# Kernel optimization log

Measured on AMD Instinct MI355X. Metric: run time of the kernel, lower is better.

Reference implementation:

```python
import jax, jax.numpy as jnp
import numpy as np

# config: nsql-350M-like, 8 layers
L, D, H, HD, FF, V, RD, MP = 8, 1024, 16, 64, 4096, 51200, 32, 4


def setup_inputs() -> dict:
    key = jax.random.key(0)
    ks = jax.random.split(key, 8)
    B, S = 1, 1024
    s = 0.02
    return {
        'idx': jax.random.randint(ks[0], (B, S), 0, V),
        'input_pos': jnp.arange(S),
        'emb': jax.random.normal(ks[1], (V, D)) * s,
        'Wqkv': jax.random.normal(ks[2], (L, 3 * D, D)) * s,
        'Wo': jax.random.normal(ks[3], (L, D, D)) * s,
        'ln1_w': jnp.ones((L, D)), 'ln1_b': jnp.zeros((L, D)),
        'fc_in_w': jax.random.normal(ks[4], (L, FF, D)) * s,
        'fc_in_b': jnp.zeros((L, FF)),
        'fc_out_w': jax.random.normal(ks[5], (L, D, FF)) * s,
        'fc_out_b': jnp.zeros((L, D)),
        'lnf_w': jnp.ones((D,)), 'lnf_b': jnp.zeros((D,)),
        'lm_w': jax.random.normal(ks[6], (V, D)) * s,
        'lm_b': jnp.zeros((V,)),
    }


def _layer_norm(x, w, b, eps=1e-5):
    mu = jnp.mean(x, axis=-1, keepdims=True)
    var = jnp.var(x, axis=-1, keepdims=True)
    return (x - mu) * jax.lax.rsqrt(var + eps) * w + b


def _new_gelu(x):
    # transformers NewGELUActivation == tanh-approx gelu
    return jax.nn.gelu(x, approximate=True)


def _sincos(input_pos):
    # create_sinusoidal_positions over rotary_dim, gathered at input_pos
    inv_freq = 1.0 / (10000.0 ** (jnp.arange(0, RD, 2, dtype=jnp.float32) / RD))
    ang = input_pos.astype(jnp.float32)[:, None] * inv_freq          # [S, RD/2]
    # repeat_interleave(..., 2, dim=-1) -> interleaved sin/cos, shape [1,S,1,RD]
    sin = jnp.repeat(jnp.sin(ang), 2, axis=-1)[None, :, None, :]
    cos = jnp.repeat(jnp.cos(ang), 2, axis=-1)[None, :, None, :]
    return sin, cos


def _rotary(x, sin, cos):
    # x: [B,S,H,HD]; GPT-J interleaved rotary on first RD dims
    xr, xp = x[..., :RD], x[..., RD:]
    x1, x2 = xr[..., ::2], xr[..., 1::2]
    rot = jnp.stack((-x2, x1), axis=-1).reshape(xr.shape)  # rotate_every_two
    return jnp.concatenate([xr * cos + rot * sin, xp], axis=-1)


def reference(idx, input_pos, emb, Wqkv, Wo, ln1_w, ln1_b, fc_in_w, fc_in_b,
              fc_out_w, fc_out_b, lnf_w, lnf_b, lm_w, lm_b):
    B, S = idx.shape
    x = emb[idx]                                        # [B,S,D]
    sin, cos = _sincos(input_pos)
    causal = jnp.tril(jnp.ones((S, S), dtype=bool))
    neg = jnp.finfo(x.dtype).min
    ld = D // MP

    def split_heads(t):
        # CodeGen _split_heads with mp_num=4: [B,S,MP,ld] -> [B,S,H,HD]
        return t.reshape(B, S, MP, H // MP, HD).reshape(B, S, H, HD)

    for l in range(L):
        h = _layer_norm(x, ln1_w[l], ln1_b[l])
        qkv = (h @ Wqkv[l].T).reshape(B, S, MP, 3 * ld)
        q, v, k = qkv[..., :ld], qkv[..., ld:2 * ld], qkv[..., 2 * ld:]  # q,v,k order!
        q = _rotary(split_heads(q), sin, cos)
        k = _rotary(split_heads(k), sin, cos)
        vh = split_heads(v)
        q, k, vh = (jnp.transpose(t, (0, 2, 1, 3)) for t in (q, k, vh))  # [B,H,S,HD]
        scores = jnp.einsum('bhqd,bhkd->bhqk', q, k) / jnp.sqrt(jnp.asarray(HD, x.dtype))
        scores = jnp.where(causal, scores, neg)
        att = jax.nn.softmax(scores, axis=-1)
        y = jnp.einsum('bhqk,bhkd->bhqd', att, vh)
        y = jnp.transpose(y, (0, 2, 1, 3)).reshape(B, S, D)
        attn_out = y @ Wo[l].T
        mlp = _new_gelu(h @ fc_in_w[l].T + fc_in_b[l]) @ fc_out_w[l].T + fc_out_b[l]
        x = attn_out + mlp + x                          # parallel block + residual

    x = _layer_norm(x, lnf_w, lnf_b)
    return x @ lm_w.T + lm_b                            # [B,S,V]
```

## Files before the change

kernel.cpp:

```cpp
#include <hip/hip_runtime.h>

#define SQ 1024
#define DIM 1024
#define NH 16
#define HDIM 64
#define FFD 4096
#define NV 51200
#define NL 8
#define LDBUF 5120
#define WELEMS ((long)(3 * DIM + DIM + FFD + FFD) * DIM)

typedef __bf16 bf16x8 __attribute__((ext_vector_type(8)));
typedef float f32x4 __attribute__((ext_vector_type(4)));

__device__ __forceinline__ unsigned short f2bf(float f) {
    union { float f; unsigned int i; } v; v.f = f;
    unsigned int r = v.i + 0x7fffu + ((v.i >> 16) & 1u);
    return (unsigned short)(r >> 16);
}
__device__ __forceinline__ float gelu_tanh(float x) {
    float x3 = x * x * x;
    return 0.5f * x * (1.0f + tanhf(0.79788456080286535588f * (x + 0.044715f * x3)));
}
__device__ __forceinline__ void cvt8(const float* __restrict__ s, unsigned short* __restrict__ d, long i) {
    float4 a = *reinterpret_cast<const float4*>(s + i);
    float4 b = *reinterpret_cast<const float4*>(s + i + 4);
    bf16x8 w;
    w[0] = (__bf16)a.x; w[1] = (__bf16)a.y; w[2] = (__bf16)a.z; w[3] = (__bf16)a.w;
    w[4] = (__bf16)b.x; w[5] = (__bf16)b.y; w[6] = (__bf16)b.z; w[7] = (__bf16)b.w;
    *reinterpret_cast<bf16x8*>(d + i) = w;
}

#define GLD16(gp, lp) __builtin_amdgcn_global_load_lds( \
    (__attribute__((address_space(1))) void*)(gp), \
    (__attribute__((address_space(3))) void*)(lp), 16, 0, 0)
#define VMCNT0 asm volatile("s_waitcnt vmcnt(0)" ::: "memory")

__global__ void cvt4_kernel(const float* __restrict__ w0, const float* __restrict__ w1,
                            const float* __restrict__ w2, const float* __restrict__ w3,
                            unsigned short* __restrict__ dst) {
    const int b = blockIdx.x;
    const float* s; long off; unsigned short* d;
    if (b < 1536)      { s = w0; d = dst;                      off = (long)b * 2048; }
    else if (b < 2048) { s = w1; d = dst + (long)3072 * 1024;  off = (long)(b - 1536) * 2048; }
    else if (b < 4096) { s = w2; d = dst + (long)4096 * 1024;  off = (long)(b - 2048) * 2048; }
    else               { s = w3; d = dst + (long)8192 * 1024;  off = (long)(b - 4096) * 2048; }
    cvt8(s, d, off + threadIdx.x * 8);
}
__global__ void cvt_kernel(const float* __restrict__ src, unsigned short* __restrict__ dst) {
    cvt8(src, dst, ((long)blockIdx.x * 256 + threadIdx.x) * 8);
}

__global__ void sincos_kernel(const int* __restrict__ pos, float2* __restrict__ sc) {
    const int t = blockIdx.x * 256 + threadIdx.x;
    if (t >= SQ * 16) return;
    const int s = t >> 4, i = t & 15;
    const float ang = (float)pos[s] * powf(10000.0f, -(float)i / 16.0f);
    sc[t] = make_float2(sinf(ang), cosf(ang));
}

__global__ void embed_kernel(const int* __restrict__ idx, const float* __restrict__ emb,
                             float* __restrict__ x) {
    const int s = blockIdx.x;
    const int d = threadIdx.x * 4;
    const int row = idx[s];
    *reinterpret_cast<float4*>(x + (long)s * DIM + d) =
        *reinterpret_cast<const float4*>(emb + (long)row * DIM + d);
}

template <bool RED>
__global__ __launch_bounds__(256) void ln_kernel(float* __restrict__ x,
                                                 const float* __restrict__ part,
                                                 const float* __restrict__ w,
                                                 const float* __restrict__ b,
                                                 unsigned short* __restrict__ out) {
    __shared__ float red[8];
    const int s = blockIdx.x, tid = threadIdx.x;
    const long fidx = (long)s * 256 + tid;
    float4 v = reinterpret_cast<const float4*>(x)[fidx];
    if (RED) {
        #pragma unroll
        for (int z = 0; z < 4; z++) {
            float4 p = reinterpret_cast<const float4*>(part + (long)z * SQ * DIM)[fidx];
            v.x += p.x; v.y += p.y; v.z += p.z; v.w += p.w;
        }
        reinterpret_cast<float4*>(x)[fidx] = v;
    }
    float sum = v.x + v.y + v.z + v.w;
    float sq = v.x * v.x + v.y * v.y + v.z * v.z + v.w * v.w;
    #pragma unroll
    for (int off = 32; off; off >>= 1) { sum += __shfl_xor(sum, off); sq += __shfl_xor(sq, off); }
    const int wid = tid >> 6, lane = tid & 63;
    if (lane == 0) { red[wid * 2] = sum; red[wid * 2 + 1] = sq; }
    __syncthreads();
    sum = red[0] + red[2] + red[4] + red[6];
    sq  = red[1] + red[3] + red[5] + red[7];
    const float mu = sum * (1.0f / DIM);
    const float var = sq * (1.0f / DIM) - mu * mu;
    const float rstd = rsqrtf(var + 1e-5f);
    const int d = tid * 4;
    float vv[4] = {v.x, v.y, v.z, v.w};
    ushort4 o;
    unsigned short* op = (unsigned short*)&o;
    #pragma unroll
    for (int j = 0; j < 4; j++)
        op[j] = f2bf((vv[j] - mu) * rstd * w[d + j] + b[d + j]);
    *reinterpret_cast<ushort4*>(out + (long)s * DIM + d) = o;
}

__global__ __launch_bounds__(256) void gemm_qkv_fcin(const unsigned short* __restrict__ A,
                                                     const unsigned short* __restrict__ B1,
                                                     const unsigned short* __restrict__ B2,
                                                     const float* __restrict__ bias,
                                                     unsigned short* __restrict__ ffout,
                                                     const float2* __restrict__ sc,
                                                     unsigned short* __restrict__ qt,
                                                     unsigned short* __restrict__ kt,
                                                     unsigned short* __restrict__ vt,
                                                     const float* __restrict__ lmsrc,
                                                     unsigned short* __restrict__ lmdst) {
    __shared__ __align__(16) unsigned short As[2][128 * 64];
    __shared__ __align__(16) unsigned short Bs[2][128 * 64];
    const int tid = threadIdx.x;
    if (blockIdx.x >= 448) {
        if (lmdst) {
            const int cb = (int)blockIdx.x - 448;
            const long stride = (long)((int)gridDim.x - 448) * 256;
            const long nlmv = (long)(NV / NL) * DIM / 8;
            for (long i = (long)cb * 256 + tid; i < nlmv; i += stride) cvt8(lmsrc, lmdst, i * 8);
        }
        return;
    }
    const int sb = (blockIdx.x & 7) * 56 + (blockIdx.x >> 3);
    const int mb = sb & 7, nb = sb >> 3;
    const int m0 = mb * 128, n0 = nb * 128;
    const int lane = tid & 63, wid = tid >> 6;
    const int l15 = lane & 15, lhi = lane >> 4;
    const int wr = wid >> 1, wc = wid & 1;
    const int sw = l15 & 7;

    const unsigned short* Bbase = B1;
    int nloc = n0;
    if (nb >= 24) { Bbase = B2; nloc = n0 - 3072; }

    f32x4 acc[4][4];
    #pragma unroll
    for (int i = 0; i < 4; i++)
        #pragma unroll
        for (int j = 0; j < 4; j++) acc[i][j] = (f32x4){0.f, 0.f, 0.f, 0.f};

    const int wbase = (tid & ~63) * 8;

    auto stage = [&](int buf, int kt_) {
        const int k0 = kt_ << 6;
        #pragma unroll
        for (int i = 0; i < 4; i++) {
            const int e = (i * 256 + tid) * 8;
            const int r = e >> 6;
            const int cs = (((e >> 3) & 7) ^ (r & 7)) * 8;
            GLD16(A + (long)(m0 + r) * DIM + k0 + cs, &As[buf][i * 2048 + wbase]);
        }
        #pragma unroll
        for (int i = 0; i < 4; i++) {
            const int e = (i * 256 + tid) * 8;
            const int r = e >> 6;
            const int cs = (((e >> 3) & 7) ^ (r & 7)) * 8;
            GLD16(Bbase + (long)(nloc + r) * 1024 + k0 + cs, &Bs[buf][i * 2048 + wbase]);
        }
    };
    auto compute = [&](int buf) {
        #pragma unroll
        for (int ks = 0; ks < 2; ks++) {
            bf16x8 af[4], bfr[4];
            #pragma unroll
            for (int mf = 0; mf < 4; mf++)
                af[mf] = *reinterpret_cast<const bf16x8*>(
                    &As[buf][(wr * 64 + mf * 16 + l15) * 64 + ((ks * 4 + lhi) ^ sw) * 8]);
            #pragma unroll
            for (int nf = 0; nf < 4; nf++)
                bfr[nf] = *reinterpret_cast<const bf16x8*>(
                    &Bs[buf][(wc * 64 + nf * 16 + l15) * 64 + ((ks * 4 + lhi) ^ sw) * 8]);
            #pragma unroll
            for (int mf = 0; mf < 4; mf++)
                #pragma unroll
                for (int nf = 0; nf < 4; nf++)
                    acc[mf][nf] = __builtin_amdgcn_mfma_f32_16x16x32_bf16(af[mf], bfr[nf], acc[mf][nf], 0, 0, 0);
        }
    };

    int cur = 0;
    stage(0, 0);
    VMCNT0; __syncthreads();
    for (int kt_ = 0; kt_ < 16; kt_++) {
        if (kt_ + 1 < 16) stage(cur ^ 1, kt_ + 1);
        compute(cur);
        if (kt_ + 1 < 16) { VMCNT0; __syncthreads(); cur ^= 1; }
    }

    if (nb < 24) {
        #pragma unroll
        for (int nf = 0; nf < 4; nf++) {
            const int col = n0 + wc * 64 + nf * 16 + l15;
            const int g = col / 768;
            const int r768 = col - g * 768;
            const int sec = r768 >> 8;
            const int off = r768 & 255;
            const int h = g * 4 + (off >> 6);
            const int d = off & 63;
            const bool isrot = (d < 32);
            const int dodd = d & 1;
            #pragma unroll
            for (int mf = 0; mf < 4; mf++) {
                #pragma unroll
                for (int j = 0; j < 4; j++) {
                    const int row = m0 + wr * 64 + mf * 16 + lhi * 4 + j;
                    float v = acc[mf][nf][j];
                    const float pv = __shfl_xor(v, 1);
                    float outv = v;
                    if (isrot && sec != 1) {
                        const float2 scv = sc[row * 16 + (d >> 1)];
                        outv = dodd ? (v * scv.y + pv * scv.x)
                                    : (v * scv.y - pv * scv.x);
                    }
                    if (sec == 0)      qt[((long)(h * SQ + row)) * HDIM + d] = f2bf(outv);
                    else if (sec == 2) kt[((long)(h * SQ + row)) * HDIM + d] = f2bf(outv);
                    else               vt[(long)h * (HDIM * SQ) + (long)d * SQ + row] = f2bf(outv);
                }
            }
        }
    } else {
        #pragma unroll
        for (int nf = 0; nf < 4; nf++) {
            const int col = n0 + wc * 64 + nf * 16 + l15;
            #pragma unroll
            for (int mf = 0; mf < 4; mf++) {
                #pragma unroll
                for (int j = 0; j < 4; j++) {
                    const int row = m0 + wr * 64 + mf * 16 + lhi * 4 + j;
                    float v = gelu_tanh(acc[mf][nf][j] + bias[col - 3072]);
                    ffout[(long)row * LDBUF + (col - 3072)] = f2bf(v);
                }
            }
        }
    }
}

__global__ __launch_bounds__(256) void attn_fcout(const unsigned short* __restrict__ qt,
                                                  const unsigned short* __restrict__ kt,
                                                  const unsigned short* __restrict__ vt,
                                                  unsigned short* __restrict__ buf,
                                                  const unsigned short* __restrict__ fcw,
                                                  const float* __restrict__ fcb,
                                                  float* __restrict__ parts,
                                                  const float* __restrict__ nw0,
                                                  const float* __restrict__ nw1,
                                                  const float* __restrict__ nw2,
                                                  const float* __restrict__ nw3,
                                                  unsigned short* __restrict__ nd) {
    __shared__ __align__(16) unsigned short smem[32768];
    const int tid = threadIdx.x, lane = tid & 63, wid = tid >> 6;
    const int l15 = lane & 15, lhi = lane >> 4;
    const int sw = l15 & 7;
    const int wbase = (tid & ~63) * 8;

    if (blockIdx.x < 256) {
        unsigned short* Ks0 = smem;
        unsigned short* Vs0 = smem + 8192;
        unsigned short* Psw = smem + 16384 + wid * 1024;
        const int h = blockIdx.x & 15;
        const int qb = 15 - ((int)blockIdx.x >> 4);
        const int q0 = qb * 64 + wid * 16;

        bf16x8 aq[2];
        {
            const unsigned short* qp = qt + ((long)(h * SQ + q0 + l15)) * HDIM;
            aq[0] = *reinterpret_cast<const bf16x8*>(qp + lhi * 8);
            aq[1] = *reinterpret_cast<const bf16x8*>(qp + 32 + lhi * 8);
        }
        f32x4 o[4];
        #pragma unroll
        for (int nf = 0; nf < 4; nf++) o[nf] = (f32x4){0.f, 0.f, 0.f, 0.f};
        float mrow[4] = {-1e30f, -1e30f, -1e30f, -1e30f};
        float lrow[4] = {0.f, 0.f, 0.f, 0.f};

        auto stageKV = [&](int b, int kv0) {
            #pragma unroll
            for (int i = 0; i < 2; i++) {
                const int e = (i * 256 + tid) * 8;
                const int r = e >> 6;
                const int cs = (((e >> 3) & 7) ^ (r & 7)) * 8;
                GLD16(kt + ((long)(h * SQ + kv0 + r)) * HDIM + cs, Ks0 + b * 4096 + i * 2048 + wbase);
                GLD16(vt + (long)h * (HDIM * SQ) + (long)r * SQ + kv0 + cs, Vs0 + b * 4096 + i * 2048 + wbase);
            }
        };

        int cur = 0;
        stageKV(0, 0);
        VMCNT0; __syncthreads();
        for (int kvt = 0; kvt <= qb; kvt++) {
            const int kv0 = kvt * 64;
            if (kvt < qb) stageKV(cur ^ 1, kv0 + 64);

            f32x4 sa[4];
            #pragma unroll
            for (int hc = 0; hc < 4; hc++) sa[hc] = (f32x4){0.f, 0.f, 0.f, 0.f};
            #pragma unroll
            for (int hc = 0; hc < 4; hc++)
                #pragma unroll
                for (int ks = 0; ks < 2; ks++) {
                    bf16x8 bk = *reinterpret_cast<const bf16x8*>(
                        Ks0 + cur * 4096 + (hc * 16 + l15) * 64 + ((ks * 4 + lhi) ^ sw) * 8);
                    sa[hc] = __builtin_amdgcn_mfma_f32_16x16x32_bf16(aq[ks], bk, sa[hc], 0, 0, 0);
                }
            float pr[4][4], mb[4];
            #pragma unroll
            for (int j = 0; j < 4; j++) {
                const int qi = q0 + lhi * 4 + j;
                #pragma unroll
                for (int hc = 0; hc < 4; hc++) {
                    const int ki = kv0 + hc * 16 + l15;
                    const float sv = sa[hc][j] * 0.125f;
                    pr[hc][j] = (ki <= qi) ? sv : -1e30f;
                }
                mb[j] = fmaxf(fmaxf(pr[0][j], pr[1][j]), fmaxf(pr[2][j], pr[3][j]));
            }
            #pragma unroll
            for (int off = 1; off < 16; off <<= 1)
                #pragma unroll
                for (int j = 0; j < 4; j++) mb[j] = fmaxf(mb[j], __shfl_xor(mb[j], off));
            float alpha[4], psum[4];
            #pragma unroll
            for (int j = 0; j < 4; j++) {
                const float mn = fmaxf(mrow[j], mb[j]);
                alpha[j] = __expf(mrow[j] - mn);
                mrow[j] = mn;
                psum[j] = 0.f;
                #pragma unroll
                for (int hc = 0; hc < 4; hc++) { pr[hc][j] = __expf(pr[hc][j] - mn); psum[j] += pr[hc][j]; }
            }
            #pragma unroll
            for (int off = 1; off < 16; off <<= 1)
                #pragma unroll
                for (int j = 0; j < 4; j++) psum[j] += __shfl_xor(psum[j], off);
            #pragma unroll
            for (int j = 0; j < 4; j++) lrow[j] = lrow[j] * alpha[j] + psum[j];
            #pragma unroll
            for (int nf = 0; nf < 4; nf++)
                #pragma unroll
                for (int j = 0; j < 4; j++) o[nf][j] *= alpha[j];
            #pragma unroll
            for (int hc = 0; hc < 4; hc++)
                #pragma unroll
                for (int j = 0; j < 4; j++) {
                    const int prow = lhi * 4 + j;
                    const int pc8 = (hc * 2 + (l15 >> 3)) ^ (prow & 7);
                    Psw[prow * 64 + pc8 * 8 + (l15 & 7)] = f2bf(pr[hc][j]);
                }
            bf16x8 ap[2];
            ap[0] = *reinterpret_cast<const bf16x8*>(Psw + l15 * 64 + ((0 + lhi) ^ sw) * 8);
            ap[1] = *reinterpret_cast<const bf16x8*>(Psw + l15 * 64 + ((4 + lhi) ^ sw) * 8);
            #pragma unroll
            for (int nf = 0; nf < 4; nf++)
                #pragma unroll
                for (int ks2 = 0; ks2 < 2; ks2++) {
                    bf16x8 bv = *reinterpret_cast<const bf16x8*>(
                        Vs0 + cur * 4096 + (nf * 16 + l15) * 64 + ((ks2 * 4 + lhi) ^ sw) * 8);
                    o[nf] = __builtin_amdgcn_mfma_f32_16x16x32_bf16(ap[ks2], bv, o[nf], 0, 0, 0);
                }
            if (kvt < qb) { VMCNT0; __syncthreads(); cur ^= 1; }
        }
        #pragma unroll
        for (int nf = 0; nf < 4; nf++)
            #pragma unroll
            for (int j = 0; j < 4; j++) {
                const int row = q0 + lhi * 4 + j;
                buf[(long)row * LDBUF + h * HDIM + nf * 16 + l15] = f2bf(o[nf][j] / lrow[j]);
            }
    } else if (blockIdx.x < 512) {
        unsigned short* As0 = smem;
        unsigned short* Bs0 = smem + 16384;
        const int b2 = (int)blockIdx.x - 256;
        const int sb = (b2 & 7) * 32 + (b2 >> 3);
        const int kz = sb & 3, nb = (sb >> 2) & 7, mb = sb >> 5;
        const int m0 = mb * 128, n0 = nb * 128;
        const int kt0 = kz * 16;
        const int wr = wid >> 1, wc = wid & 1;
        const unsigned short* Aff = buf + DIM;

        f32x4 acc[4][4];
        #pragma unroll
        for (int i = 0; i < 4; i++)
            #pragma unroll
            for (int j = 0; j < 4; j++) acc[i][j] = (f32x4){0.f, 0.f, 0.f, 0.f};

        auto stage = [&](int bf_, int kt_) {
            const int k0 = kt_ << 6;
            #pragma unroll
            for (int i = 0; i < 4; i++) {
                const int e = (i * 256 + tid) * 8;
                const int r = e >> 6;
                const int cs = (((e >> 3) & 7) ^ (r & 7)) * 8;
                GLD16(Aff + (long)(m0 + r) * LDBUF + k0 + cs, As0 + bf_ * 8192 + i * 2048 + wbase);
                GLD16(fcw + (long)(n0 + r) * FFD + k0 + cs, Bs0 + bf_ * 8192 + i * 2048 + wbase);
            }
        };
        auto compute = [&](int bf_) {
            #pragma unroll
            for (int ks = 0; ks < 2; ks++) {
                bf16x8 af[4], bfr[4];
                #pragma unroll
                for (int mf = 0; mf < 4; mf++)
                    af[mf] = *reinterpret_cast<const bf16x8*>(
                        As0 + bf_ * 8192 + (wr * 64 + mf * 16 + l15) * 64 + ((ks * 4 + lhi) ^ sw) * 8);
                #pragma unroll
                for (int nf = 0; nf < 4; nf++)
                    bfr[nf] = *reinterpret_cast<const bf16x8*>(
                        Bs0 + bf_ * 8192 + (wc * 64 + nf * 16 + l15) * 64 + ((ks * 4 + lhi) ^ sw) * 8);
                #pragma unroll
                for (int mf = 0; mf < 4; mf++)
                    #pragma unroll
                    for (int nf = 0; nf < 4; nf++)
                        acc[mf][nf] = __builtin_amdgcn_mfma_f32_16x16x32_bf16(af[mf], bfr[nf], acc[mf][nf], 0, 0, 0);
            }
        };

        int cur = 0;
        stage(0, kt0);
        VMCNT0; __syncthreads();
        for (int t = 0; t < 16; t++) {
            if (t + 1 < 16) stage(cur ^ 1, kt0 + t + 1);
            compute(cur);
            if (t + 1 < 16) { VMCNT0; __syncthreads(); cur ^= 1; }
        }

        float* P = parts + (long)kz * SQ * DIM;
        #pragma unroll
        for (int nf = 0; nf < 4; nf++) {
            const int col = n0 + wc * 64 + nf * 16 + l15;
            const float bv = (kz == 0) ? fcb[col] : 0.f;
            #pragma unroll
            for (int mf = 0; mf < 4; mf++) {
                #pragma unroll
                for (int j = 0; j < 4; j++) {
                    const int row = m0 + wr * 64 + mf * 16 + lhi * 4 + j;
                    P[(long)row * DIM + col] = acc[mf][nf][j] + bv;
                }
            }
        }
    } else {
        if (nd) {
            const int cb = (int)blockIdx.x - 512;
            const long stride = (long)((int)gridDim.x - 512) * 256;
            const long base = (long)cb * 256 + tid;
            const long n0v = (long)3072 * 1024 / 8, n1v = (long)1024 * 1024 / 8;
            const long n2v = (long)4096 * 1024 / 8, n3v = (long)4096 * 1024 / 8;
            for (long i = base; i < n0v; i += stride) cvt8(nw0, nd, i * 8);
            unsigned short* d1 = nd + n0v * 8;
            for (long i = base; i < n1v; i += stride) cvt8(nw1, d1, i * 8);
            unsigned short* d2 = d1 + n1v * 8;
            for (long i = base; i < n2v; i += stride) cvt8(nw2, d2, i * 8);
            unsigned short* d3 = d2 + n2v * 8;
            for (long i = base; i < n3v; i += stride) cvt8(nw3, d3, i * 8);
        }
    }
}

__global__ __launch_bounds__(256) void wo_rmw(const unsigned short* __restrict__ buf,
                                              const unsigned short* __restrict__ wo,
                                              float* __restrict__ parts) {
    __shared__ __align__(16) unsigned short As[2][128 * 64];
    __shared__ __align__(16) unsigned short Bs[2][128 * 64];
    const int tid = threadIdx.x;
    const int sb = (blockIdx.x & 7) * 32 + (blockIdx.x >> 3);
    const int kz = sb & 3, nb = (sb >> 2) & 7, mb = sb >> 5;
    const int m0 = mb * 128, n0 = nb * 128;
    const int kt0 = kz * 4;
    const int lane = tid & 63, wid = tid >> 6;
    const int l15 = lane & 15, lhi = lane >> 4;
    const int wr = wid >> 1, wc = wid & 1;
    const int sw = l15 & 7;
    const int wbase = (tid & ~63) * 8;

    f32x4 acc[4][4];
    #pragma unroll
    for (int i = 0; i < 4; i++)
        #pragma unroll
        for (int j = 0; j < 4; j++) acc[i][j] = (f32x4){0.f, 0.f, 0.f, 0.f};

    auto stage = [&](int bf_, int kt_) {
        const int k0 = kt_ << 6;
        #pragma unroll
        for (int i = 0; i < 4; i++) {
            const int e = (i * 256 + tid) * 8;
            const int r = e >> 6;
            const int cs = (((e >> 3) & 7) ^ (r & 7)) * 8;
            GLD16(buf + (long)(m0 + r) * LDBUF + k0 + cs, &As[bf_][i * 2048 + wbase]);
            GLD16(wo + (long)(n0 + r) * DIM + k0 + cs, &Bs[bf_][i * 2048 + wbase]);
        }
    };
    auto compute = [&](int bf_) {
        #pragma unroll
        for (int ks = 0; ks < 2; ks++) {
            bf16x8 af[4], bfr[4];
            #pragma unroll
            for (int mf = 0; mf < 4; mf++)
                af[mf] = *reinterpret_cast<const bf16x8*>(
                    &As[bf_][(wr * 64 + mf * 16 + l15) * 64 + ((ks * 4 + lhi) ^ sw) * 8]);
            #pragma unroll
            for (int nf = 0; nf < 4; nf++)
                bfr[nf] = *reinterpret_cast<const bf16x8*>(
                    &Bs[bf_][(wc * 64 + nf * 16 + l15) * 64 + ((ks * 4 + lhi) ^ sw) * 8]);
            #pragma unroll
            for (int mf = 0; mf < 4; mf++)
                #pragma unroll
                for (int nf = 0; nf < 4; nf++)
                    acc[mf][nf] = __builtin_amdgcn_mfma_f32_16x16x32_bf16(af[mf], bfr[nf], acc[mf][nf], 0, 0, 0);
        }
    };

    int cur = 0;
    stage(0, kt0);
    VMCNT0; __syncthreads();
    for (int t = 0; t < 4; t++) {
        if (t + 1 < 4) stage(cur ^ 1, kt0 + t + 1);
        compute(cur);
        if (t + 1 < 4) { VMCNT0; __syncthreads(); cur ^= 1; }
    }

    float* P = parts + (long)kz * SQ * DIM;
    #pragma unroll
    for (int nf = 0; nf < 4; nf++) {
        const int col = n0 + wc * 64 + nf * 16 + l15;
        #pragma unroll
        for (int mf = 0; mf < 4; mf++) {
            #pragma unroll
            for (int j = 0; j < 4; j++) {
                const int row = m0 + wr * 64 + mf * 16 + lhi * 4 + j;
                P[(long)row * DIM + col] += acc[mf][nf][j];
            }
        }
    }
}

__global__ __launch_bounds__(512) void gemm256p8(const unsigned short* __restrict__ A,
                                                 const unsigned short* __restrict__ B,
                                                 const float* __restrict__ bias,
                                                 float* __restrict__ C) {
    __shared__ __align__(16) unsigned short As[2][2][128 * 64];
    __shared__ __align__(16) unsigned short Bs[2][2][128 * 64];
    const int tid = threadIdx.x;
    const int nwg = gridDim.x, qch = nwg >> 3;
    const int sb = (blockIdx.x & 7) * qch + (blockIdx.x >> 3);
    const int mb = sb & 3, nb = sb >> 2;
    const int m0 = mb * 256, n0 = nb * 256;
    const int lane = tid & 63, wid = tid >> 6;
    const int l15 = lane & 15, lhi = lane >> 4;
    const int wm = wid >> 2, wn = wid & 3;
    const int sw = l15 & 7;
    const int wbase = (tid & ~63) * 8;

    f32x4 acc[8][4];
    #pragma unroll
    for (int i = 0; i < 8; i++)
        #pragma unroll
        for (int j = 0; j < 4; j++) acc[i][j] = (f32x4){0.f, 0.f, 0.f, 0.f};

    auto stageA = [&](int kt, int hh) {
        const int k0 = kt << 6;
        unsigned short* dst = &As[kt & 1][hh][0];
        #pragma unroll
        for (int i = 0; i < 2; i++) {
            const int e = (i * 512 + tid) * 8;
            const int r = e >> 6;
            const int cs = (((e >> 3) & 7) ^ (r & 7)) * 8;
            GLD16(A + (long)(m0 + hh * 128 + r) * 1024 + k0 + cs, dst + i * 4096 + wbase);
        }
    };
    auto stageB = [&](int kt, int hh) {
        const int k0 = kt << 6;
        unsigned short* dst = &Bs[kt & 1][hh][0];
        #pragma unroll
        for (int i = 0; i < 2; i++) {
            const int e = (i * 512 + tid) * 8;
            const int r = e >> 6;
            const int cs = (((e >> 3) & 7) ^ (r & 7)) * 8;
            GLD16(B + (long)(n0 + hh * 128 + r) * 1024 + k0 + cs, dst + i * 4096 + wbase);
        }
    };

    bf16x8 afA[4][2], bf0[2][2], bf1[2][2];
    auto ldA = [&](int buf, int hh) {
        #pragma unroll
        for (int mi = 0; mi < 4; mi++) {
            const int row = wm * 64 + mi * 16 + l15;
            #pragma unroll
            for (int ks = 0; ks < 2; ks++)
                afA[mi][ks] = *reinterpret_cast<const bf16x8*>(
                    &As[buf][hh][row * 64 + (((ks * 4 + lhi) ^ sw) * 8)]);
        }
    };
    auto ldB = [&](int buf, int hh, bf16x8 (&bfr)[2][2]) {
        #pragma unroll
        for (int ni = 0; ni < 2; ni++) {
            const int row = wn * 32 + ni * 16 + l15;
            #pragma unroll
            for (int ks = 0; ks < 2; ks++)
                bfr[ni][ks] = *reinterpret_cast<const bf16x8*>(
                    &Bs[buf][hh][row * 64 + (((ks * 4 + lhi) ^ sw) * 8)]);
        }
    };
    auto mfma16 = [&](int mh, int nh, bf16x8 (&bfr)[2][2]) {
        __builtin_amdgcn_s_setprio(1);
        #pragma unroll
        for (int mi = 0; mi < 4; mi++)
            #pragma unroll
            for (int ni = 0; ni < 2; ni++)
                #pragma unroll
                for (int ks = 0; ks < 2; ks++)
                    acc[mh * 4 + mi][nh * 2 + ni] = __builtin_amdgcn_mfma_f32_16x16x32_bf16(
                        afA[mi][ks], bfr[ni][ks], acc[mh * 4 + mi][nh * 2 + ni], 0, 0, 0);
        __builtin_amdgcn_s_setprio(0);
    };

#define BAR()   __builtin_amdgcn_s_barrier()
#define LGKM()  asm volatile("s_waitcnt lgkmcnt(0)" ::: "memory")
#define VM6()   asm volatile("s_waitcnt vmcnt(6)" ::: "memory")

    stageA(0, 0); stageB(0, 0); stageB(0, 1); stageA(0, 1);
    stageA(1, 0); stageB(1, 0); stageB(1, 1);
    VM6();
    BAR();

    for (int it = 0; it < 8; it++) {
        const int e = 2 * it, o = 2 * it + 1;
        const bool more = (it + 1 < 8);
        ldA(0, 0); ldB(0, 0, bf0);
        stageA(o, 1);
        BAR(); LGKM(); mfma16(0, 0, bf0); BAR();
        ldB(0, 1, bf1);
        if (more) stageA(e + 2, 0);
        BAR(); LGKM(); mfma16(0, 1, bf1); BAR();
        ldA(0, 1);
        if (more) stageB(e + 2, 0);
        BAR(); LGKM(); mfma16(1, 1, bf1); BAR();
        if (more) stageB(e + 2, 1);
        if (more) { VM6(); } else { VMCNT0; }
        BAR(); LGKM(); mfma16(1, 0, bf0); BAR();
        ldA(1, 0); ldB(1, 0, bf0);
        if (more) stageA(e + 2, 1);
        BAR(); LGKM(); mfma16(0, 0, bf0); BAR();
        ldB(1, 1, bf1);
        if (more) stageA(o + 2, 0);
        BAR(); LGKM(); mfma16(0, 1, bf1); BAR();
        ldA(1, 1);
        if (more) stageB(o + 2, 0);
        BAR(); LGKM(); mfma16(1, 1, bf1); BAR();
        if (more) { stageB(o + 2, 1); VM6(); }
        BAR(); LGKM(); mfma16(1, 0, bf0); BAR();
    }
#undef BAR
#undef LGKM
#undef VM6

    #pragma unroll
    for (int nf = 0; nf < 4; nf++) {
        const int col = n0 + (nf < 2 ? wn * 32 + nf * 16 : 128 + wn * 32 + (nf - 2) * 16) + l15;
        const float bv = bias[col];
        #pragma unroll
        for (int mf = 0; mf < 8; mf++) {
            const int rowb = m0 + (mf < 4 ? wm * 64 + mf * 16 : 128 + wm * 64 + (mf - 4) * 16) + lhi * 4;
            #pragma unroll
            for (int j = 0; j < 4; j++)
                C[(long)(rowb + j) * NV + col] = acc[mf][nf][j] + bv;
        }
    }
}

__global__ __launch_bounds__(512) void gemm256(const unsigned short* __restrict__ A,
                                               const unsigned short* __restrict__ B,
                                               const float* __restrict__ bias,
                                               float* __restrict__ C, int coff) {
    __shared__ __align__(16) unsigned short As[2][256 * 64];
    __shared__ __align__(16) unsigned short Bs[2][256 * 64];
    const int tid = threadIdx.x;
    const int nwg = gridDim.x, qch = nwg >> 3;
    const int sb = (blockIdx.x & 7) * qch + (blockIdx.x >> 3);
    const int mb = sb & 3, nb = sb >> 2;
    const int m0 = mb * 256, n0 = coff + nb * 256;
    const int lane = tid & 63, wid = tid >> 6;
    const int l15 = lane & 15, lhi = lane >> 4;
    const int wm = wid >> 2, wn = wid & 3;
    const int sw = l15 & 7;

    f32x4 acc[8][4];
    #pragma unroll
    for (int i = 0; i < 8; i++)
        #pragma unroll
        for (int j = 0; j < 4; j++) acc[i][j] = (f32x4){0.f, 0.f, 0.f, 0.f};

    const int wbase = (tid & ~63) * 8;

    auto stage = [&](int buf, int kt) {
        const int k0 = kt << 6;
        #pragma unroll
        for (int i = 0; i < 4; i++) {
            const int e = (i * 512 + tid) * 8;
            const int r = e >> 6;
            const int cs = (((e >> 3) & 7) ^ (r & 7)) * 8;
            GLD16(A + (long)(m0 + r) * 1024 + k0 + cs, &As[buf][i * 4096 + wbase]);
            GLD16(B + (long)(n0 + r) * 1024 + k0 + cs, &Bs[buf][i * 4096 + wbase]);
        }
    };
    auto compute = [&](int buf) {
        #pragma unroll
        for (int ks = 0; ks < 2; ks++) {
            bf16x8 af[8], bfr[4];
            #pragma unroll
            for (int mf = 0; mf < 8; mf++)
                af[mf] = *reinterpret_cast<const bf16x8*>(
                    &As[buf][(wm * 128 + mf * 16 + l15) * 64 + ((ks * 4 + lhi) ^ sw) * 8]);
            #pragma unroll
            for (int nf = 0; nf < 4; nf++)
                bfr[nf] = *reinterpret_cast<const bf16x8*>(
                    &Bs[buf][(wn * 64 + nf * 16 + l15) * 64 + ((ks * 4 + lhi) ^ sw) * 8]);
            #pragma unroll
            for (int mf = 0; mf < 8; mf++)
                #pragma unroll
                for (int nf = 0; nf < 4; nf++)
                    acc[mf][nf] = __builtin_amdgcn_mfma_f32_16x16x32_bf16(af[mf], bfr[nf], acc[mf][nf], 0, 0, 0);
        }
    };

    int cur = 0;
    stage(0, 0);
    VMCNT0; __syncthreads();
    for (int kt = 0; kt < 16; kt++) {
        if (kt < 15) stage(cur ^ 1, kt + 1);
        compute(cur);
        if (kt < 15) { VMCNT0; __syncthreads(); cur ^= 1; }
    }

    #pragma unroll
    for (int nf = 0; nf < 4; nf++) {
        const int col = n0 + wn * 64 + nf * 16 + l15;
        const float bv = bias[col];
        #pragma unroll
        for (int mf = 0; mf < 8; mf++) {
            #pragma unroll
            for (int j = 0; j < 4; j++) {
                const int row = m0 + wm * 128 + mf * 16 + lhi * 4 + j;
                C[(long)row * NV + col] = acc[mf][nf][j] + bv;
            }
        }
    }
}

extern "C" void kernel_launch(void* const* d_in, const int* in_sizes, int n_in,
                              void* d_out, int out_size, void* d_ws, size_t ws_size,
                              hipStream_t stream) {
    const int* idx    = (const int*)d_in[0];
    const int* pos    = (const int*)d_in[1];
    const float* emb  = (const float*)d_in[2];
    const float* Wqkv = (const float*)d_in[3];
    const float* Wo   = (const float*)d_in[4];
    const float* ln1w = (const float*)d_in[5];
    const float* ln1b = (const float*)d_in[6];
    const float* fciw = (const float*)d_in[7];
    const float* fcib = (const float*)d_in[8];
    const float* fcow = (const float*)d_in[9];
    const float* fcob = (const float*)d_in[10];
    const float* lnfw = (const float*)d_in[11];
    const float* lnfb = (const float*)d_in[12];
    const float* lmw  = (const float*)d_in[13];
    const float* lmb  = (const float*)d_in[14];

    const long tailBytes = (long)SQ * DIM * 4 + (long)4 * SQ * DIM * 4 + (long)SQ * DIM * 2
                         + (long)3 * NH * SQ * HDIM * 2 + (long)SQ * LDBUF * 2 + (long)SQ * 16 * 8;
    const long bigBytes  = 2 * WELEMS * 2 + (long)NV * DIM * 2 + tailBytes;
    const bool big = (long)ws_size >= bigBytes + (1 << 20);

    char* ws = (char*)d_ws;
    unsigned short *wbufA, *wbufB, *lmbuf;
    if (big) {
        wbufA = (unsigned short*)ws; ws += WELEMS * 2;
        wbufB = (unsigned short*)ws; ws += WELEMS * 2;
        lmbuf = (unsigned short*)ws; ws += (long)NV * DIM * 2;
    } else {
        wbufA = (unsigned short*)ws; ws += (long)NV * DIM * 2;
        wbufB = wbufA;
        lmbuf = wbufA;
    }
    float* x           = (float*)ws;          ws += (long)SQ * DIM * 4;
    float* parts       = (float*)ws;          ws += (long)4 * SQ * DIM * 4;
    unsigned short* h  = (unsigned short*)ws; ws += (long)SQ * DIM * 2;
    unsigned short* qt = (unsigned short*)ws; ws += (long)NH * SQ * HDIM * 2;
    unsigned short* kt = (unsigned short*)ws; ws += (long)NH * SQ * HDIM * 2;
    unsigned short* vt = (unsigned short*)ws; ws += (long)NH * SQ * HDIM * 2;
    unsigned short* buf= (unsigned short*)ws; ws += (long)SQ * LDBUF * 2;
    float2* sc         = (float2*)ws;         ws += (long)SQ * 16 * 8;

    auto wq = [&](unsigned short* wb) { return wb; };
    auto wo_ = [&](unsigned short* wb) { return wb + (long)3072 * 1024; };
    auto wfi = [&](unsigned short* wb) { return wb + (long)4096 * 1024; };
    auto wfo = [&](unsigned short* wb) { return wb + (long)8192 * 1024; };

    sincos_kernel<<<64, 256, 0, stream>>>(pos, sc);
    embed_kernel<<<SQ, 256, 0, stream>>>(idx, emb, x);
    cvt4_kernel<<<6144, 256, 0, stream>>>(Wqkv, Wo, fciw, fcow, wbufA);

    for (int l = 0; l < NL; l++) {
        unsigned short* wb = (l & 1) ? wbufB : wbufA;
        unsigned short* wn = (l & 1) ? wbufA : wbufB;

        if (!big && l > 0)
            cvt4_kernel<<<6144, 256, 0, stream>>>(Wqkv + (long)l * 3 * DIM * DIM,
                                                  Wo   + (long)l * DIM * DIM,
                                                  fciw + (long)l * FFD * DIM,
                                                  fcow + (long)l * DIM * FFD, wb);

        if (l == 0) ln_kernel<false><<<SQ, 256, 0, stream>>>(x, nullptr, ln1w, ln1b, h);
        else ln_kernel<true><<<SQ, 256, 0, stream>>>(x, parts, ln1w + (long)l * DIM, ln1b + (long)l * DIM, h);

        gemm_qkv_fcin<<<704, 256, 0, stream>>>(h, wq(wb), wfi(wb), fcib + (long)l * FFD,
                                               buf + DIM, sc, qt, kt, vt,
                                               big ? lmw + (long)l * (NV / NL) * DIM : nullptr,
                                               big ? lmbuf + (long)l * (NV / NL) * DIM : nullptr);
        if (big) {
            const int nl = l + 1;
            attn_fcout<<<1024, 256, 0, stream>>>(qt, kt, vt, buf, wfo(wb),
                                                 fcob + (long)l * DIM, parts,
                                                 (nl < NL) ? Wqkv + (long)nl * 3 * DIM * DIM : nullptr,
                                                 (nl < NL) ? Wo   + (long)nl * DIM * DIM : nullptr,
                                                 (nl < NL) ? fciw + (long)nl * FFD * DIM : nullptr,
                                                 (nl < NL) ? fcow + (long)nl * DIM * FFD : nullptr,
                                                 (nl < NL) ? wn : nullptr);
        } else {
            attn_fcout<<<512, 256, 0, stream>>>(qt, kt, vt, buf, wfo(wb),
                                                fcob + (long)l * DIM, parts,
                                                nullptr, nullptr, nullptr, nullptr, nullptr);
        }
        wo_rmw<<<256, 256, 0, stream>>>(buf, wo_(wb), parts);
    }
    if (!big) cvt_kernel<<<25600, 256, 0, stream>>>(lmw, lmbuf);
    ln_kernel<true><<<SQ, 256, 0, stream>>>(x, parts, lnfw, lnfb, h);
    gemm256p8<<<600, 512, 0, stream>>>(h, lmbuf, lmb, (float*)d_out);
    gemm256<<<200, 512, 0, stream>>>(h, lmbuf, lmb, (float*)d_out, 38400);
}
```

Baseline: 983.7 us.

## Read attention K/V directly from global and run LM head with one GEMM kernel

The attention branch of attn_fcout no longer stages K and V tiles into LDS with double buffering and barriers. Each wave now loads its MFMA B operands straight from global memory, which drops the per-tile syncs but gives up LDS reuse and the swizzled layout. Separately, the LM-head tail is no longer split between gemm256p8 and a plain gemm256. All 800 blocks now go through gemm256p8, and the gemm256 kernel is deleted.

```diff
diff --git a/kernel.cpp b/kernel.cpp
--- a/kernel.cpp
+++ b/kernel.cpp
@@ -264,9 +264,7 @@
     const int wbase = (tid & ~63) * 8;
 
     if (blockIdx.x < 256) {
-        unsigned short* Ks0 = smem;
-        unsigned short* Vs0 = smem + 8192;
-        unsigned short* Psw = smem + 16384 + wid * 1024;
+        unsigned short* Psw = smem + wid * 1024;
         const int h = blockIdx.x & 15;
         const int qb = 15 - ((int)blockIdx.x >> 4);
         const int q0 = qb * 64 + wid * 16;
@@ -283,24 +281,11 @@
         float mrow[4] = {-1e30f, -1e30f, -1e30f, -1e30f};
         float lrow[4] = {0.f, 0.f, 0.f, 0.f};
 
-        auto stageKV = [&](int b, int kv0) {
-            #pragma unroll
-            for (int i = 0; i < 2; i++) {
-                const int e = (i * 256 + tid) * 8;
-                const int r = e >> 6;
-                const int cs = (((e >> 3) & 7) ^ (r & 7)) * 8;
-                GLD16(kt + ((long)(h * SQ + kv0 + r)) * HDIM + cs, Ks0 + b * 4096 + i * 2048 + wbase);
-                GLD16(vt + (long)h * (HDIM * SQ) + (long)r * SQ + kv0 + cs, Vs0 + b * 4096 + i * 2048 + wbase);
-            }
-        };
-
-        int cur = 0;
-        stageKV(0, 0);
-        VMCNT0; __syncthreads();
+        const unsigned short* kbase = kt + (long)h * SQ * HDIM;
+        const unsigned short* vbase = vt + (long)h * (HDIM * SQ);
+
         for (int kvt = 0; kvt <= qb; kvt++) {
             const int kv0 = kvt * 64;
-            if (kvt < qb) stageKV(cur ^ 1, kv0 + 64);
-
             f32x4 sa[4];
             #pragma unroll
             for (int hc = 0; hc < 4; hc++) sa[hc] = (f32x4){0.f, 0.f, 0.f, 0.f};
@@ -309,7 +294,7 @@
                 #pragma unroll
                 for (int ks = 0; ks < 2; ks++) {
                     bf16x8 bk = *reinterpret_cast<const bf16x8*>(
-                        Ks0 + cur * 4096 + (hc * 16 + l15) * 64 + ((ks * 4 + lhi) ^ sw) * 8);
+                        kbase + (long)(kv0 + hc * 16 + l15) * HDIM + ks * 32 + lhi * 8);
                     sa[hc] = __builtin_amdgcn_mfma_f32_16x16x32_bf16(aq[ks], bk, sa[hc], 0, 0, 0);
                 }
             float pr[4][4], mb[4];
@@ -364,10 +349,9 @@
                 #pragma unroll
                 for (int ks2 = 0; ks2 < 2; ks2++) {
                     bf16x8 bv = *reinterpret_cast<const bf16x8*>(
-                        Vs0 + cur * 4096 + (nf * 16 + l15) * 64 + ((ks2 * 4 + lhi) ^ sw) * 8);
+                        vbase + (long)(nf * 16 + l15) * SQ + kv0 + ks2 * 32 + lhi * 8);
                     o[nf] = __builtin_amdgcn_mfma_f32_16x16x32_bf16(ap[ks2], bv, o[nf], 0, 0, 0);
                 }
-            if (kvt < qb) { VMCNT0; __syncthreads(); cur ^= 1; }
         }
         #pragma unroll
         for (int nf = 0; nf < 4; nf++)
@@ -676,85 +660,6 @@
     }
 }
 
-__global__ __launch_bounds__(512) void gemm256(const unsigned short* __restrict__ A,
-                                               const unsigned short* __restrict__ B,
-                                               const float* __restrict__ bias,
-                                               float* __restrict__ C, int coff) {
-    __shared__ __align__(16) unsigned short As[2][256 * 64];
-    __shared__ __align__(16) unsigned short Bs[2][256 * 64];
-    const int tid = threadIdx.x;
-    const int nwg = gridDim.x, qch = nwg >> 3;
-    const int sb = (blockIdx.x & 7) * qch + (blockIdx.x >> 3);
-    const int mb = sb & 3, nb = sb >> 2;
-    const int m0 = mb * 256, n0 = coff + nb * 256;
-    const int lane = tid & 63, wid = tid >> 6;
-    const int l15 = lane & 15, lhi = lane >> 4;
-    const int wm = wid >> 2, wn = wid & 3;
-    const int sw = l15 & 7;
-
-    f32x4 acc[8][4];
-    #pragma unroll
-    for (int i = 0; i < 8; i++)
-        #pragma unroll
-        for (int j = 0; j < 4; j++) acc[i][j] = (f32x4){0.f, 0.f, 0.f, 0.f};
-
-    const int wbase = (tid & ~63) * 8;
-
-    auto stage = [&](int buf, int kt) {
-        const int k0 = kt << 6;
-        #pragma unroll
-        for (int i = 0; i < 4; i++) {
-            const int e = (i * 512 + tid) * 8;
-            const int r = e >> 6;
-            const int cs = (((e >> 3) & 7) ^ (r & 7)) * 8;
-            GLD16(A + (long)(m0 + r) * 1024 + k0 + cs, &As[buf][i * 4096 + wbase]);
-            GLD16(B + (long)(n0 + r) * 1024 + k0 + cs, &Bs[buf][i * 4096 + wbase]);
-        }
-    };
-    auto compute = [&](int buf) {
-        #pragma unroll
-        for (int ks = 0; ks < 2; ks++) {
-            bf16x8 af[8], bfr[4];
-            #pragma unroll
-            for (int mf = 0; mf < 8; mf++)
-                af[mf] = *reinterpret_cast<const bf16x8*>(
-                    &As[buf][(wm * 128 + mf * 16 + l15) * 64 + ((ks * 4 + lhi) ^ sw) * 8]);
-            #pragma unroll
-            for (int nf = 0; nf < 4; nf++)
-                bfr[nf] = *reinterpret_cast<const bf16x8*>(
-                    &Bs[buf][(wn * 64 + nf * 16 + l15) * 64 + ((ks * 4 + lhi) ^ sw) * 8]);
-            #pragma unroll
-            for (int mf = 0; mf < 8; mf++)
-                #pragma unroll
-                for (int nf = 0; nf < 4; nf++)
-                    acc[mf][nf] = __builtin_amdgcn_mfma_f32_16x16x32_bf16(af[mf], bfr[nf], acc[mf][nf], 0, 0, 0);
-        }
-    };
-
-    int cur = 0;
-    stage(0, 0);
-    VMCNT0; __syncthreads();
-    for (int kt = 0; kt < 16; kt++) {
-        if (kt < 15) stage(cur ^ 1, kt + 1);
-        compute(cur);
-        if (kt < 15) { VMCNT0; __syncthreads(); cur ^= 1; }
-    }
-
-    #pragma unroll
-    for (int nf = 0; nf < 4; nf++) {
-        const int col = n0 + wn * 64 + nf * 16 + l15;
-        const float bv = bias[col];
-        #pragma unroll
-        for (int mf = 0; mf < 8; mf++) {
-            #pragma unroll
-            for (int j = 0; j < 4; j++) {
-                const int row = m0 + wm * 128 + mf * 16 + lhi * 4 + j;
-                C[(long)row * NV + col] = acc[mf][nf][j] + bv;
-            }
-        }
-    }
-}
-
 extern "C" void kernel_launch(void* const* d_in, const int* in_sizes, int n_in,
                               void* d_out, int out_size, void* d_ws, size_t ws_size,
                               hipStream_t stream) {
@@ -843,6 +748,5 @@
     }
     if (!big) cvt_kernel<<<25600, 256, 0, stream>>>(lmw, lmbuf);
     ln_kernel<true><<<SQ, 256, 0, stream>>>(x, parts, lnfw, lnfb, h);
-    gemm256p8<<<600, 512, 0, stream>>>(h, lmbuf, lmb, (float*)d_out);
-    gemm256<<<200, 512, 0, stream>>>(h, lmbuf, lmb, (float*)d_out, 38400);
-}
+    gemm256p8<<<800, 512, 0, stream>>>(h, lmbuf, lmb, (float*)d_out);
+}
```

Measured after the change: 1.015 ms. 3.2% more time.
